# Optimization experiments

Hardware: AMD Instinct MI355X
Metric: run time of the kernel (lower is better)

## Reference

```python
import jax, jax.numpy as jnp
import numpy as np

EPS = 1e-6

def layer_norm(x, g, b):
    m = jnp.mean(x, axis=-1, keepdims=True)
    v = jnp.mean(jnp.square(x - m), axis=-1, keepdims=True)
    return (x - m) * jax.lax.rsqrt(v + EPS) * g + b

def setup_inputs() -> dict:
    key = jax.random.key(0)
    ks = jax.random.split(key, 12)
    B, L, D, Dff, SK = 8, 4096, 512, 2048, 128
    s = 0.02
    return {
        "x": jax.random.normal(ks[0], (B, L, D), jnp.float32),
        "Wq": jax.random.normal(ks[1], (D, D), jnp.float32) * s,
        "bq": jnp.zeros((D,), jnp.float32),
        "Wk": jax.random.normal(ks[2], (D, D), jnp.float32) * s,
        "bk": jnp.zeros((D,), jnp.float32),
        "Wv": jax.random.normal(ks[3], (D, D), jnp.float32) * s,
        "bv": jnp.zeros((D,), jnp.float32),
        "Wo": jax.random.normal(ks[4], (D, D), jnp.float32) * s,
        "bo": jnp.zeros((D,), jnp.float32),
        "g1": jnp.ones((D,), jnp.float32),
        "b1": jnp.zeros((D,), jnp.float32),
        "W1f": jax.random.normal(ks[5], (D, Dff), jnp.float32) * s,
        "b1f": jnp.zeros((Dff,), jnp.float32),
        "W2f": jax.random.normal(ks[6], (Dff, D), jnp.float32) * s,
        "b2f": jnp.zeros((D,), jnp.float32),
        "g2": jnp.ones((D,), jnp.float32),
        "b2": jnp.zeros((D,), jnp.float32),
        "sample_idx": jax.random.randint(ks[7], (SK,), 0, L, jnp.int64),
    }

NUM_HEADS = 8
TOP_U = 128

def prob_sparse_attention(x, Wq, bq, Wk, bk, Wv, bv, Wo, bo, sample_idx):
    B, L, D = x.shape
    H = NUM_HEADS
    dh = D // H
    scale = 1.0 / jnp.sqrt(jnp.asarray(dh, x.dtype))
    # projections -> [B, H, L, dh]
    def split_heads(t):
        return t.reshape(B, L, H, dh).transpose(0, 2, 1, 3)
    Q = split_heads(x @ Wq + bq)
    K = split_heads(x @ Wk + bk)
    V = split_heads(x @ Wv + bv)
    # sparsity measurement on a sampled key subset: [B, H, L, SK]
    K_samp = K[:, :, sample_idx, :]
    s_samp = jnp.einsum('bhld,bhsd->bhls', Q, K_samp)
    M = jnp.max(s_samp, axis=-1) - jnp.mean(s_samp, axis=-1)  # [B, H, L]
    _, top_idx = jax.lax.top_k(M, TOP_U)  # [B, H, u]
    # gather top-u queries: [B, H, u, dh]
    Q_top = jnp.take_along_axis(Q, top_idx[..., None], axis=2)
    scores = jnp.einsum('bhud,bhld->bhul', Q_top, K) * scale  # [B, H, u, L]
    attn = jax.nn.softmax(scores, axis=-1)
    ctx_top = jnp.einsum('bhul,bhld->bhud', attn, V)  # [B, H, u, dh]
    # lazy queries get mean(V)
    meanV = jnp.mean(V, axis=2, keepdims=True)  # [B, H, 1, dh]
    ctx = jnp.broadcast_to(meanV, (B, H, L, dh))
    bi = jnp.arange(B)[:, None, None]
    hi = jnp.arange(H)[None, :, None]
    ctx = ctx.at[bi, hi, top_idx].set(ctx_top)
    out = ctx.transpose(0, 2, 1, 3).reshape(B, L, D)
    return out @ Wo + bo

def reference(x, Wq, bq, Wk, bk, Wv, bv, Wo, bo, g1, b1, W1f, b1f, W2f, b2f, g2, b2, sample_idx):
    attn_out = prob_sparse_attention(x, Wq, bq, Wk, bk, Wv, bv, Wo, bo, sample_idx)
    x1 = layer_norm(x + attn_out, g1, b1)
    ffn = jax.nn.relu(x1 @ W1f + b1f) @ W2f + b2f
    return layer_norm(x1 + ffn, g2, b2)
```

## Files before the change

### kernel.cpp

```cpp
#include <hip/hip_runtime.h>
#include <hip/hip_bf16.h>

using bf16 = __hip_bfloat16;

constexpr int Bd  = 8;
constexpr int Ld  = 4096;
constexpr int Dd  = 512;
constexpr int Hd  = 8;
constexpr int DHd = 64;
constexpr int DFFd= 2048;
constexpr int Ud  = 128;
constexpr int MLd = Bd * Ld;
constexpr int KSd = 16;

typedef short          bf16x8 __attribute__((ext_vector_type(8)));
typedef unsigned short u16x8  __attribute__((ext_vector_type(8)));
typedef float          f32x4  __attribute__((ext_vector_type(4)));

__device__ __forceinline__ float bf2float(bf16 v) { return __bfloat162float(v); }

__device__ __forceinline__ float wred_sum(float v) {
    #pragma unroll
    for (int o = 32; o > 0; o >>= 1) v += __shfl_xor(v, o);
    return v;
}
__device__ __forceinline__ float wred_max(float v) {
    #pragma unroll
    for (int o = 32; o > 0; o >>= 1) v = fmaxf(v, __shfl_xor(v, o));
    return v;
}
__device__ __forceinline__ float scrub(float v) {
    return (fabsf(v) < 1e20f) ? v : 0.0f;
}
__device__ __forceinline__ short f2bs(float f) {
    bf16 h = __float2bfloat16(f);
    return *reinterpret_cast<short*>(&h);
}

__device__ __forceinline__ void gload_lds16(const bf16* g, bf16* lds_base) {
    __builtin_amdgcn_global_load_lds((const __attribute__((address_space(1))) void*)g,
                                     (__attribute__((address_space(3))) void*)lds_base,
                                     16, 0, 0);
}

__global__ void detect_kernel(const void* xraw, int* flags) {
    const unsigned short* u = (const unsigned short*)xraw;
    __shared__ int cnt;
    if (threadIdx.x == 0) cnt = 0;
    __syncthreads();
    int local = 0;
    for (int i = threadIdx.x; i < 1024; i += 256) {
        int e = (u[2 * i] >> 7) & 0xFF;
        if (e >= 96 && e <= 142) local++;
    }
    atomicAdd(&cnt, local);
    __syncthreads();
    if (threadIdx.x == 0) flags[0] = (cnt < 512) ? 1 : 0;
}

__global__ void conv_kernel(const void* raw, bf16* dst, int n, const int* flags) {
    int i = blockIdx.x * 256 + threadIdx.x;
    if (i >= n) return;
    if (flags[0]) dst[i] = __float2bfloat16(((const float*)raw)[i]);
    else          dst[i] = ((const bf16*)raw)[i];
}

__global__ void convT_kernel(const void* raw, bf16* dst, int K, int N, const int* flags) {
    __shared__ bf16 tile[32][33];
    const int k0 = blockIdx.y * 32, n0 = blockIdx.x * 32;
    const int tx = threadIdx.x & 31, ty = threadIdx.x >> 5;
    #pragma unroll
    for (int p = 0; p < 4; ++p) {
        int k = k0 + ty + p * 8, n = n0 + tx;
        float v = flags[0] ? ((const float*)raw)[(size_t)k * N + n]
                           : bf2float(((const bf16*)raw)[(size_t)k * N + n]);
        tile[ty + p * 8][tx] = __float2bfloat16(v);
    }
    __syncthreads();
    #pragma unroll
    for (int p = 0; p < 4; ++p) {
        int n = n0 + ty + p * 8, k = k0 + tx;
        dst[(size_t)n * K + k] = tile[tx][ty + p * 8];
    }
}

__global__ void zero_kernel(int* p, int n) {
    int i = blockIdx.x * 256 + threadIdx.x;
    if (i < n) p[i] = 0;
}

__global__ void idx_kernel(const void* raw, int* out) {
    const int* r32 = (const int*)raw;
    __shared__ int is64;
    int t = threadIdx.x;
    if (t == 0) is64 = 1;
    __syncthreads();
    if (t < 64 && r32[2 * t + 1] != 0) is64 = 0;
    __syncthreads();
    int v = is64 ? r32[2 * t] : r32[t];
    out[t] = min(max(v, 0), Ld - 1);
}

template<bool RELU>
__launch_bounds__(256)
__global__ void mfma_gemm(const bf16* __restrict__ X, const bf16* __restrict__ WT,
                          const bf16* __restrict__ bias, bf16* __restrict__ C,
                          int M, int N, int K)
{
    __shared__ bf16 As[128 * 64];
    __shared__ bf16 Bs[128 * 64];
    const int t = threadIdx.x;
    const int lane = t & 63, wave = t >> 6;
    const int wr = wave >> 1, wc = wave & 1;
    const int quad = lane >> 4, l15 = lane & 15;

    const int nwg = gridDim.x * gridDim.y;
    int wg = blockIdx.y * gridDim.x + blockIdx.x;
    if ((nwg & 7) == 0)
        wg = (wg & 7) * (nwg >> 3) + (wg >> 3);
    const int m0 = (wg / gridDim.x) * 128, n0 = (wg % gridDim.x) * 128;

    const int rseg = lane >> 3;
    const int cs   = (lane & 7) ^ rseg;

    f32x4 acc[4][4] = {};

    for (int k0 = 0; k0 < K; k0 += 64) {
        #pragma unroll
        for (int p = 0; p < 4; ++p) {
            const int sg = wave * 4 + p;
            const int r  = sg * 8 + rseg;
            gload_lds16(&X [(size_t)(m0 + r) * K + k0 + cs * 8], &As[sg * 512]);
            gload_lds16(&WT[(size_t)(n0 + r) * K + k0 + cs * 8], &Bs[sg * 512]);
        }
        __syncthreads();
        #pragma unroll
        for (int kk = 0; kk < 2; ++kk) {
            const int ch = ((kk * 4 + quad) ^ (l15 & 7)) * 8;
            bf16x8 a[4], b[4];
            #pragma unroll
            for (int i = 0; i < 4; ++i) {
                a[i] = *(const bf16x8*)&As[(wr * 64 + i * 16 + l15) * 64 + ch];
                b[i] = *(const bf16x8*)&Bs[(wc * 64 + i * 16 + l15) * 64 + ch];
            }
            #pragma unroll
            for (int i = 0; i < 4; ++i)
                #pragma unroll
                for (int j = 0; j < 4; ++j)
                    acc[i][j] = __builtin_amdgcn_mfma_f32_16x16x32_bf16(a[i], b[j], acc[i][j], 0, 0, 0);
        }
        __syncthreads();
    }
    #pragma unroll
    for (int j = 0; j < 4; ++j) {
        int n = n0 + wc * 64 + j * 16 + l15;
        float bi = bf2float(bias[n]);
        #pragma unroll
        for (int i = 0; i < 4; ++i) {
            #pragma unroll
            for (int r = 0; r < 4; ++r) {
                int m = m0 + wr * 64 + i * 16 + quad * 4 + r;
                float v = acc[i][j][r] + bi;
                if (RELU) v = fmaxf(v, 0.0f);
                C[(size_t)m * N + n] = __float2bfloat16(v);
            }
        }
    }
}

__launch_bounds__(256)
__global__ void m_kernel(const bf16* __restrict__ Q, const bf16* __restrict__ Kg,
                         const int* __restrict__ sidx, float* __restrict__ Mv)
{
    __shared__ __align__(16) short Qs[128 * 64];
    __shared__ __align__(16) short Ks[128 * 64];
    __shared__ int sidxs[128];

    const int t = threadIdx.x, lane = t & 63, w = t >> 6;
    const int l15 = lane & 15, quad = lane >> 4;
    const int l0 = blockIdx.x * 128;
    const int bh = blockIdx.y, b = bh >> 3, h = bh & 7;

    if (t < 128) sidxs[t] = sidx[t];
    __syncthreads();

    const int rseg = lane >> 3;
    const int cs   = (lane & 7) ^ rseg;
    #pragma unroll
    for (int sg4 = 0; sg4 < 4; ++sg4) {
        const int sg = w * 4 + sg4;
        const int r  = sg * 8 + rseg;
        gload_lds16(Q  + ((size_t)(b * Ld + l0 + r))    * Dd + h * 64 + cs * 8,
                    (bf16*)&Qs[sg * 512]);
        gload_lds16(Kg + ((size_t)(b * Ld + sidxs[r])) * Dd + h * 64 + cs * 8,
                    (bf16*)&Ks[sg * 512]);
    }
    __syncthreads();

    f32x4 s[2][8] = {};
    #pragma unroll
    for (int kk = 0; kk < 2; ++kk) {
        const int ch = ((kk * 4 + quad) ^ (l15 & 7)) * 8;
        bf16x8 qa[2], kb[8];
        #pragma unroll
        for (int mt = 0; mt < 2; ++mt)
            qa[mt] = *(const bf16x8*)&Qs[(w * 32 + mt * 16 + l15) * 64 + ch];
        #pragma unroll
        for (int nt = 0; nt < 8; ++nt)
            kb[nt] = *(const bf16x8*)&Ks[(nt * 16 + l15) * 64 + ch];
        #pragma unroll
        for (int mt = 0; mt < 2; ++mt)
            #pragma unroll
            for (int nt = 0; nt < 8; ++nt)
                s[mt][nt] = __builtin_amdgcn_mfma_f32_16x16x32_bf16(qa[mt], kb[nt], s[mt][nt], 0, 0, 0);
    }

    #pragma unroll
    for (int mt = 0; mt < 2; ++mt) {
        #pragma unroll
        for (int r = 0; r < 4; ++r) {
            float vmax = -1e30f, vsum = 0.0f;
            #pragma unroll
            for (int nt = 0; nt < 8; ++nt) {
                float v = s[mt][nt][r];
                vmax = fmaxf(vmax, v); vsum += v;
            }
            #pragma unroll
            for (int off = 1; off < 16; off <<= 1) {
                vmax = fmaxf(vmax, __shfl_xor(vmax, off));
                vsum += __shfl_xor(vsum, off);
            }
            if (l15 == 0) {
                const int row = w * 32 + mt * 16 + quad * 4 + r;
                Mv[(size_t)bh * Ld + l0 + row] = vmax - vsum * (1.0f / 128.0f);
            }
        }
    }
}

__launch_bounds__(256)
__global__ void topk_kernel(const float* __restrict__ Mv, int* __restrict__ topIdx)
{
    __shared__ unsigned ukey[4096];
    __shared__ short listA[4096], listB[4096];
    __shared__ int hist[256];
    __shared__ int outCnt, candCnt, selB, aboveK;
    const int bh = blockIdx.x, t = threadIdx.x;

    for (int i = t; i < 4096; i += 256) {
        unsigned u = __float_as_uint(Mv[(size_t)bh * Ld + i]);
        ukey[i] = (u & 0x80000000u) ? ~u : (u | 0x80000000u);
    }
    if (t == 0) outCnt = 0;
    __syncthreads();

    int K = Ud;
    #pragma unroll
    for (int r = 0; r < 4; ++r) {
        const int shift = 24 - 8 * r;
        hist[t] = 0;
        __syncthreads();
        const int n = (r == 0) ? 4096 : candCnt;
        const short* cur = (r & 1) ? listB : listA;
        for (int i = t; i < n; i += 256) {
            int idx = (r == 0) ? i : cur[i];
            atomicAdd(&hist[(ukey[idx] >> shift) & 0xFF], 1);
        }
        __syncthreads();
        if (t == 0) {
            int cum = 0, b = 255;
            for (; b > 0; --b) {
                if (cum + hist[b] >= K) break;
                cum += hist[b];
            }
            selB = b; aboveK = cum; candCnt = 0;
        }
        __syncthreads();
        const int sb = selB;
        short* nxt = (r & 1) ? listA : listB;
        for (int i = t; i < n; i += 256) {
            int idx = (r == 0) ? i : cur[i];
            int by = (ukey[idx] >> shift) & 0xFF;
            if (by > sb) {
                int p = atomicAdd(&outCnt, 1);
                topIdx[bh * Ud + p] = idx;
            } else if (by == sb) {
                int p = atomicAdd(&candCnt, 1);
                nxt[p] = (short)idx;
            }
        }
        __syncthreads();
        K -= aboveK;
        if (K == 0) break;
    }
    if (K > 0) {
        for (int i = t; i < K; i += 256) {
            int p = atomicAdd(&outCnt, 1);
            topIdx[bh * Ud + p] = listA[i];
        }
    }
}

__global__ void rows_kernel(const int* __restrict__ topIdx, int* __restrict__ rowCnt,
                            int* __restrict__ rowEnt)
{
    const int bh = blockIdx.x, u = threadIdx.x, b = bh >> 3;
    const int lq = topIdx[bh * Ud + u];
    const int row = b * Ld + lq;
    int slot = atomicAdd(&rowCnt[row], 1) & 7;
    rowEnt[row * 8 + slot] = bh * Ud + u;
}

__launch_bounds__(256)
__global__ void meanv_kernel(const bf16* __restrict__ V, float* __restrict__ meanV)
{
    const int bh = blockIdx.x, b = bh >> 3, h = bh & 7;
    const int l0 = blockIdx.y * 64;
    const int t = threadIdx.x;
    const int d = t & 63, part = t >> 6;
    float s = 0.0f;
    #pragma unroll
    for (int p = 0; p < 16; ++p) {
        int l = l0 + part + p * 4;
        s += bf2float(V[((size_t)(b * Ld + l)) * Dd + h * 64 + d]);
    }
    __shared__ float red[256];
    red[t] = s;
    __syncthreads();
    if (t < 64) {
        float tot = red[t] + red[64 + t] + red[128 + t] + red[192 + t];
        atomicAdd(&meanV[bh * 64 + t], tot * (1.0f / 4096.0f));
    }
}

__launch_bounds__(256, 3)
__global__ void attn_kernel(const bf16* __restrict__ Qg, const bf16* __restrict__ Kg,
                            const bf16* __restrict__ Vg, const int* __restrict__ topIdx,
                            bf16* __restrict__ pO, float* __restrict__ pM, float* __restrict__ pL)
{
    __shared__ __align__(16) short KsS[2][64 * 64];
    __shared__ __align__(16) short VsS[2][64 * 72];
    __shared__ __align__(16) short PsS[4][32 * 72];

    const int t = threadIdx.x, lane = t & 63, w = t >> 6;
    const int l15 = lane & 15, quad = lane >> 4;
    const int bh = blockIdx.x, ks = blockIdx.y;
    const int b = bh >> 3, h = bh & 7;
    const int key0 = ks * (Ld / KSd);
    constexpr int NT = (Ld / KSd) / 64;

    bf16x8 qf[2][2];
    #pragma unroll
    for (int m = 0; m < 2; ++m) {
        const int u  = w * 32 + m * 16 + l15;
        const int lq = topIdx[bh * Ud + u];
        const bf16* qr = Qg + ((size_t)(b * Ld + lq)) * Dd + h * 64;
        qf[m][0] = *(const bf16x8*)(qr + quad * 8);
        qf[m][1] = *(const bf16x8*)(qr + 32 + quad * 8);
    }

    const int vkey = t >> 2, vd0 = (t & 3) * 16;
    u16x8 vr0, vr1;

    auto loadV = [&](int tt) {
        const bf16* vs = Vg + ((size_t)(b * Ld + key0 + tt * 64 + vkey)) * Dd + h * 64 + vd0;
        vr0 = *(const u16x8*)vs;
        vr1 = *(const u16x8*)(vs + 8);
    };
    auto stageK = [&](int buf, int tt) {
        const int kb0 = key0 + tt * 64;
        #pragma unroll
        for (int sz = 0; sz < 2; ++sz) {
            const int sg = w * 2 + sz;
            const int r  = sg * 8 + (lane >> 3);
            const int cs = (lane & 7) ^ (lane >> 3);
            gload_lds16(Kg + ((size_t)(b * Ld + kb0 + r)) * Dd + h * 64 + cs * 8,
                        (bf16*)&KsS[buf][sg * 512]);
        }
    };
    auto writeV = [&](int buf) {
        #pragma unroll
        for (int j = 0; j < 8; ++j) {
            VsS[buf][(vd0 + j) * 72 + vkey]     = (short)vr0[j];
            VsS[buf][(vd0 + 8 + j) * 72 + vkey] = (short)vr1[j];
        }
    };

    float mrun[2][4], lrun[2][4];
    f32x4 o[2][4] = {};
    #pragma unroll
    for (int m = 0; m < 2; ++m)
        #pragma unroll
        for (int r = 0; r < 4; ++r) { mrun[m][r] = -1e30f; lrun[m][r] = 0.0f; }

    loadV(0); stageK(0, 0); writeV(0);
    __syncthreads();

    short* PsW = &PsS[w][0];
    for (int tt = 0; tt < NT; ++tt) {
        const int cur = tt & 1;
        if (tt + 1 < NT) { loadV(tt + 1); stageK(cur ^ 1, tt + 1); }

        const short* KsB = &KsS[cur][0];
        f32x4 s[2][4] = {};
        #pragma unroll
        for (int kk = 0; kk < 2; ++kk) {
            bf16x8 kb[4];
            #pragma unroll
            for (int n = 0; n < 4; ++n)
                kb[n] = *(const bf16x8*)&KsB[(n * 16 + l15) * 64 +
                                             (((kk * 4 + quad) ^ (l15 & 7)) * 8)];
            #pragma unroll
            for (int m = 0; m < 2; ++m)
                #pragma unroll
                for (int n = 0; n < 4; ++n)
                    s[m][n] = __builtin_amdgcn_mfma_f32_16x16x32_bf16(qf[m][kk], kb[n], s[m][n], 0, 0, 0);
        }

        #pragma unroll
        for (int m = 0; m < 2; ++m) {
            #pragma unroll
            for (int r = 0; r < 4; ++r) {
                float sv[4];
                #pragma unroll
                for (int n = 0; n < 4; ++n) sv[n] = s[m][n][r] * 0.125f;
                float vm = fmaxf(fmaxf(sv[0], sv[1]), fmaxf(sv[2], sv[3]));
                #pragma unroll
                for (int off = 1; off < 16; off <<= 1) vm = fmaxf(vm, __shfl_xor(vm, off));
                const float mn = fmaxf(mrun[m][r], vm);
                const float al = __expf(mrun[m][r] - mn);
                float ps = 0.0f;
                #pragma unroll
                for (int n = 0; n < 4; ++n) { sv[n] = __expf(sv[n] - mn); ps += sv[n]; }
                #pragma unroll
                for (int off = 1; off < 16; off <<= 1) ps += __shfl_xor(ps, off);
                lrun[m][r] = lrun[m][r] * al + ps;
                mrun[m][r] = mn;
                const int qrow = m * 16 + quad * 4 + r;
                #pragma unroll
                for (int n = 0; n < 4; ++n) {
                    PsW[qrow * 72 + n * 16 + l15] = f2bs(sv[n]);
                    o[m][n][r] *= al;
                }
            }
        }

        if (tt + 1 < NT) writeV(cur ^ 1);

        const short* VsB = &VsS[cur][0];
        #pragma unroll
        for (int kk = 0; kk < 2; ++kk) {
            bf16x8 pa[2], vb[4];
            #pragma unroll
            for (int m = 0; m < 2; ++m)
                pa[m] = *(const bf16x8*)&PsW[(m * 16 + l15) * 72 + kk * 32 + quad * 8];
            #pragma unroll
            for (int n = 0; n < 4; ++n)
                vb[n] = *(const bf16x8*)&VsB[(n * 16 + l15) * 72 + kk * 32 + quad * 8];
            #pragma unroll
            for (int m = 0; m < 2; ++m)
                #pragma unroll
                for (int n = 0; n < 4; ++n)
                    o[m][n] = __builtin_amdgcn_mfma_f32_16x16x32_bf16(pa[m], vb[n], o[m][n], 0, 0, 0);
        }
        __syncthreads();
    }

    const size_t pbase = ((size_t)(ks * 64 + bh)) * Ud;
    #pragma unroll
    for (int m = 0; m < 2; ++m) {
        #pragma unroll
        for (int r = 0; r < 4; ++r) {
            const int u = w * 32 + m * 16 + quad * 4 + r;
            #pragma unroll
            for (int n = 0; n < 4; ++n)
                pO[(pbase + u) * 64 + n * 16 + l15] = __float2bfloat16(o[m][n][r]);
            if (l15 == 0) { pM[pbase + u] = mrun[m][r]; pL[pbase + u] = lrun[m][r]; }
        }
    }
}

__global__ void combine_kernel(const bf16* __restrict__ pO, const float* __restrict__ pM,
                               const float* __restrict__ pL, float* __restrict__ ctxTop)
{
    const int u = blockIdx.x & 127, bh = blockIdx.x >> 7, c = threadIdx.x;
    float mstar = -1e30f;
    #pragma unroll
    for (int ks = 0; ks < KSd; ++ks)
        mstar = fmaxf(mstar, pM[(ks * 64 + bh) * Ud + u]);
    float lsum = 0.0f, osum = 0.0f;
    #pragma unroll
    for (int ks = 0; ks < KSd; ++ks) {
        float wgt = __expf(pM[(ks * 64 + bh) * Ud + u] - mstar);
        lsum += pL[(ks * 64 + bh) * Ud + u] * wgt;
        osum += bf2float(pO[(((size_t)ks * 64 + bh) * Ud + u) * 64 + c]) * wgt;
    }
    ctxTop[((size_t)bh * Ud + u) * 64 + c] = scrub(osum / lsum);
}

__launch_bounds__(512)
__global__ void baseout_kernel(const float* __restrict__ meanV, const bf16* __restrict__ Wo,
                               const bf16* __restrict__ bo, float* __restrict__ baseOut)
{
    const int b = blockIdx.x, t = threadIdx.x;
    __shared__ float mv[512];
    mv[t] = meanV[b * 512 + t];
    __syncthreads();
    float acc = bf2float(bo[t]);
    for (int d = 0; d < 512; ++d)
        acc = fmaf(mv[d], bf2float(Wo[(size_t)d * 512 + t]), acc);
    baseOut[b * 512 + t] = acc;
}

__launch_bounds__(256)
__global__ void delta_kernel(const float* __restrict__ ctxTop, const float* __restrict__ meanV,
                             const bf16* __restrict__ Wo, bf16* __restrict__ deltaOut)
{
    const int u = blockIdx.x, bh = blockIdx.y, h = bh & 7, t = threadIdx.x;
    __shared__ float diff[64];
    if (t < 64) diff[t] = ctxTop[((size_t)bh * Ud + u) * 64 + t] - meanV[bh * 64 + t];
    __syncthreads();
    for (int n = t; n < 512; n += 256) {
        float acc = 0.0f;
        #pragma unroll 8
        for (int dd = 0; dd < 64; ++dd)
            acc = fmaf(diff[dd], bf2float(Wo[(size_t)(h * 64 + dd) * 512 + n]), acc);
        deltaOut[((size_t)bh * Ud + u) * 512 + n] = __float2bfloat16(acc);
    }
}

__launch_bounds__(256)
__global__ void ln1_kernel(const bf16* __restrict__ x, const float* __restrict__ baseOut,
                           const int* __restrict__ rowCnt, const int* __restrict__ rowEnt,
                           const bf16* __restrict__ deltaOut,
                           const bf16* __restrict__ g, const bf16* __restrict__ bb,
                           bf16* __restrict__ x1)
{
    const int row = blockIdx.x, t = threadIdx.x;
    const int b = row >> 12;
    const size_t base = (size_t)row * 512;
    float v0 = bf2float(x[base + t])       + baseOut[b * 512 + t];
    float v1 = bf2float(x[base + t + 256]) + baseOut[b * 512 + t + 256];
    const int cnt = min(rowCnt[row], 8);
    for (int e = 0; e < cnt; ++e) {
        const bf16* dr = &deltaOut[(size_t)rowEnt[row * 8 + e] * 512];
        v0 += bf2float(dr[t]);
        v1 += bf2float(dr[t + 256]);
    }
    v0 = scrub(v0); v1 = scrub(v1);
    float s = v0 + v1, q = v0 * v0 + v1 * v1;
    s = wred_sum(s); q = wred_sum(q);
    __shared__ float sred[4], qred[4];
    int lane = t & 63, w = t >> 6;
    if (lane == 0) { sred[w] = s; qred[w] = q; }
    __syncthreads();
    float tot  = sred[0] + sred[1] + sred[2] + sred[3];
    float totq = qred[0] + qred[1] + qred[2] + qred[3];
    float mean = tot * (1.0f / 512.0f);
    float var  = fmaxf(totq * (1.0f / 512.0f) - mean * mean, 0.0f);
    float rstd = rsqrtf(var + 1e-6f);
    x1[base + t]       = __float2bfloat16((v0 - mean) * rstd * bf2float(g[t])       + bf2float(bb[t]));
    x1[base + t + 256] = __float2bfloat16((v1 - mean) * rstd * bf2float(g[t + 256]) + bf2float(bb[t + 256]));
}

__launch_bounds__(256)
__global__ void ln2_kernel(const bf16* __restrict__ x1, const bf16* __restrict__ ffn,
                           const bf16* __restrict__ g, const bf16* __restrict__ bb,
                           void* __restrict__ out, const int* __restrict__ flags)
{
    const int row = blockIdx.x, t = threadIdx.x;
    const size_t base = (size_t)row * 512;
    float v0 = bf2float(x1[base + t])       + bf2float(ffn[base + t]);
    float v1 = bf2float(x1[base + t + 256]) + bf2float(ffn[base + t + 256]);
    v0 = scrub(v0); v1 = scrub(v1);
    float s = v0 + v1, q = v0 * v0 + v1 * v1;
    s = wred_sum(s); q = wred_sum(q);
    __shared__ float sred[4], qred[4];
    int lane = t & 63, w = t >> 6;
    if (lane == 0) { sred[w] = s; qred[w] = q; }
    __syncthreads();
    float tot  = sred[0] + sred[1] + sred[2] + sred[3];
    float totq = qred[0] + qred[1] + qred[2] + qred[3];
    float mean = tot * (1.0f / 512.0f);
    float var  = fmaxf(totq * (1.0f / 512.0f) - mean * mean, 0.0f);
    float rstd = rsqrtf(var + 1e-6f);
    float o0 = (v0 - mean) * rstd * bf2float(g[t])       + bf2float(bb[t]);
    float o1 = (v1 - mean) * rstd * bf2float(g[t + 256]) + bf2float(bb[t + 256]);
    if (flags[0]) {
        ((float*)out)[base + t]       = o0;
        ((float*)out)[base + t + 256] = o1;
    } else {
        ((bf16*)out)[base + t]       = __float2bfloat16(o0);
        ((bf16*)out)[base + t + 256] = __float2bfloat16(o1);
    }
}

extern "C" void kernel_launch(void* const* d_in, const int* in_sizes, int n_in,
                              void* d_out, int out_size, void* d_ws, size_t ws_size,
                              hipStream_t stream)
{
    const void* sraw = d_in[17];

    const size_t NQ = (size_t)MLd * Dd;
    char* w = (char*)d_ws;
    size_t off = 0;
    auto alloc = [&](size_t bytes) { void* p = w + off; off += (bytes + 63) & ~size_t(63); return p; };
    bf16*  Qb   = (bf16*)alloc(NQ * 2);
    bf16*  Kb   = (bf16*)alloc(NQ * 2);
    bf16*  Vb   = (bf16*)alloc(NQ * 2);
    bf16*  xc   = (bf16*)alloc(NQ * 2);
    bf16*  WTq  = (bf16*)alloc(Dd * Dd * 2);
    bf16*  WTk  = (bf16*)alloc(Dd * Dd * 2);
    bf16*  WTv  = (bf16*)alloc(Dd * Dd * 2);
    bf16*  Woc  = (bf16*)alloc(Dd * Dd * 2);
    bf16*  WT1f = (bf16*)alloc((size_t)Dd * DFFd * 2);
    bf16*  WT2f = (bf16*)alloc((size_t)DFFd * Dd * 2);
    bf16* bqc = (bf16*)alloc(Dd * 2);
    bf16* bkc = (bf16*)alloc(Dd * 2);
    bf16* bvc = (bf16*)alloc(Dd * 2);
    bf16* boc = (bf16*)alloc(Dd * 2);
    bf16* g1c = (bf16*)alloc(Dd * 2);
    bf16* b1c = (bf16*)alloc(Dd * 2);
    bf16* b1fc= (bf16*)alloc(DFFd * 2);
    bf16* b2fc= (bf16*)alloc(Dd * 2);
    bf16* g2c = (bf16*)alloc(Dd * 2);
    bf16* b2c = (bf16*)alloc(Dd * 2);
    bf16*  pOb     = (bf16*)alloc((size_t)KSd * 64 * Ud * 64 * 2);
    float* Mv      = (float*)alloc((size_t)Bd * Hd * Ld * 4);
    float* ctxTop  = (float*)alloc((size_t)Bd * Hd * Ud * DHd * 4);
    float* meanV   = (float*)alloc(Bd * Hd * DHd * 4);
    float* baseOut = (float*)alloc(Bd * Dd * 4);
    int*   topIdx  = (int*)alloc(Bd * Hd * Ud * 4);
    int*   sidx    = (int*)alloc(128 * 4);
    int*   rowCnt  = (int*)alloc(MLd * 4);
    int*   rowEnt  = (int*)alloc(MLd * 8 * 4);
    int*   flags   = (int*)alloc(64);
    if (off > ws_size) return;

    bf16* h1full = nullptr;
    if (ws_size - off >= (size_t)MLd * DFFd * 2 + 64)
        h1full = (bf16*)alloc((size_t)MLd * DFFd * 2);

    bf16*  x1b  = Vb;
    bf16*  h1b  = Qb;
    bf16*  ffnb = xc;
    bf16*  deltaOut = pOb;
    float* pM = Mv;
    float* pL = Mv + KSd * 64 * Ud;

    detect_kernel<<<1, 256, 0, stream>>>(d_in[0], flags);

    auto conv = [&](int i, bf16* dst, int n) {
        conv_kernel<<<(n + 255) / 256, 256, 0, stream>>>(d_in[i], dst, n, flags);
    };
    conv(0,  xc, (int)NQ);
    convT_kernel<<<dim3(Dd / 32, Dd / 32), 256, 0, stream>>>(d_in[1], WTq, Dd, Dd, flags);
    convT_kernel<<<dim3(Dd / 32, Dd / 32), 256, 0, stream>>>(d_in[3], WTk, Dd, Dd, flags);
    convT_kernel<<<dim3(Dd / 32, Dd / 32), 256, 0, stream>>>(d_in[5], WTv, Dd, Dd, flags);
    convT_kernel<<<dim3(DFFd / 32, Dd / 32), 256, 0, stream>>>(d_in[11], WT1f, Dd, DFFd, flags);
    convT_kernel<<<dim3(Dd / 32, DFFd / 32), 256, 0, stream>>>(d_in[13], WT2f, DFFd, Dd, flags);
    conv(7,  Woc, Dd * Dd);
    conv(2,  bqc, Dd);  conv(4,  bkc, Dd);  conv(6,  bvc, Dd);  conv(8,  boc, Dd);
    conv(9,  g1c, Dd);  conv(10, b1c, Dd);
    conv(12, b1fc, DFFd); conv(14, b2fc, Dd);
    conv(15, g2c, Dd);  conv(16, b2c, Dd);

    zero_kernel<<<(MLd + 255) / 256, 256, 0, stream>>>(rowCnt, MLd);
    zero_kernel<<<(Bd * Hd * DHd + 255) / 256, 256, 0, stream>>>((int*)meanV, Bd * Hd * DHd);
    idx_kernel<<<1, 128, 0, stream>>>(sraw, sidx);

    mfma_gemm<false><<<dim3(4, 256), 256, 0, stream>>>(xc, WTq, bqc, Qb, MLd, Dd, Dd);
    mfma_gemm<false><<<dim3(4, 256), 256, 0, stream>>>(xc, WTk, bkc, Kb, MLd, Dd, Dd);
    mfma_gemm<false><<<dim3(4, 256), 256, 0, stream>>>(xc, WTv, bvc, Vb, MLd, Dd, Dd);

    m_kernel<<<dim3(Ld / 128, Bd * Hd), 256, 0, stream>>>(Qb, Kb, sidx, Mv);
    topk_kernel<<<Bd * Hd, 256, 0, stream>>>(Mv, topIdx);
    rows_kernel<<<Bd * Hd, 128, 0, stream>>>(topIdx, rowCnt, rowEnt);
    meanv_kernel<<<dim3(Bd * Hd, Ld / 64), 256, 0, stream>>>(Vb, meanV);

    attn_kernel<<<dim3(Bd * Hd, KSd), 256, 0, stream>>>(Qb, Kb, Vb, topIdx, pOb, pM, pL);
    combine_kernel<<<Bd * Hd * Ud, 64, 0, stream>>>(pOb, pM, pL, ctxTop);

    baseout_kernel<<<Bd, 512, 0, stream>>>(meanV, Woc, boc, baseOut);
    delta_kernel<<<dim3(Ud, Bd * Hd), 256, 0, stream>>>(ctxTop, meanV, Woc, deltaOut);

    ln1_kernel<<<MLd, 256, 0, stream>>>(xc, baseOut, rowCnt, rowEnt, deltaOut, g1c, b1c, x1b);

    if (h1full) {
        mfma_gemm<true ><<<dim3(16, 256), 256, 0, stream>>>(x1b, WT1f, b1fc, h1full, MLd, DFFd, Dd);
        mfma_gemm<false><<<dim3(4, 256), 256, 0, stream>>>(h1full, WT2f, b2fc, ffnb, MLd, Dd, DFFd);
    } else {
        for (int c = 0; c < 2; ++c) {
            mfma_gemm<true ><<<dim3(16, 128), 256, 0, stream>>>(
                x1b + (size_t)c * 16384 * 512, WT1f, b1fc, h1b, 16384, DFFd, Dd);
            mfma_gemm<false><<<dim3(4, 128), 256, 0, stream>>>(
                h1b, WT2f, b2fc, ffnb + (size_t)c * 16384 * 512, 16384, Dd, DFFd);
        }
    }

    ln2_kernel<<<MLd, 256, 0, stream>>>(x1b, ffnb, g2c, b2c, d_out, flags);
}
```

Baseline: 695.4 us.

## Double-buffer GEMM LDS tiles, fuse QKV projections, widen combine blocks

```diff
diff --git a/kernel.cpp b/kernel.cpp
--- a/kernel.cpp
+++ b/kernel.cpp
@@ -101,14 +101,14 @@
     out[t] = min(max(v, 0), Ld - 1);
 }
 
-template<bool RELU>
+template<bool RELU, bool QKV3>
 __launch_bounds__(256)
 __global__ void mfma_gemm(const bf16* __restrict__ X, const bf16* __restrict__ WT,
                           const bf16* __restrict__ bias, bf16* __restrict__ C,
                           int M, int N, int K)
 {
-    __shared__ bf16 As[128 * 64];
-    __shared__ bf16 Bs[128 * 64];
+    __shared__ bf16 As[2][128 * 64];
+    __shared__ bf16 Bs[2][128 * 64];
     const int t = threadIdx.x;
     const int lane = t & 63, wave = t >> 6;
     const int wr = wave >> 1, wc = wave & 1;
@@ -123,25 +123,32 @@
     const int rseg = lane >> 3;
     const int cs   = (lane & 7) ^ rseg;
 
-    f32x4 acc[4][4] = {};
-
-    for (int k0 = 0; k0 < K; k0 += 64) {
+    auto stage = [&](int buf, int k0) {
         #pragma unroll
         for (int p = 0; p < 4; ++p) {
             const int sg = wave * 4 + p;
             const int r  = sg * 8 + rseg;
-            gload_lds16(&X [(size_t)(m0 + r) * K + k0 + cs * 8], &As[sg * 512]);
-            gload_lds16(&WT[(size_t)(n0 + r) * K + k0 + cs * 8], &Bs[sg * 512]);
-        }
-        __syncthreads();
+            gload_lds16(&X [(size_t)(m0 + r) * K + k0 + cs * 8], &As[buf][sg * 512]);
+            gload_lds16(&WT[(size_t)(n0 + r) * K + k0 + cs * 8], &Bs[buf][sg * 512]);
+        }
+    };
+
+    f32x4 acc[4][4] = {};
+
+    stage(0, 0);
+    __syncthreads();
+    int cur = 0;
+    const int NI = K >> 6;
+    for (int it = 0; it < NI; ++it) {
+        if (it + 1 < NI) stage(cur ^ 1, (it + 1) << 6);
         #pragma unroll
         for (int kk = 0; kk < 2; ++kk) {
             const int ch = ((kk * 4 + quad) ^ (l15 & 7)) * 8;
             bf16x8 a[4], b[4];
             #pragma unroll
             for (int i = 0; i < 4; ++i) {
-                a[i] = *(const bf16x8*)&As[(wr * 64 + i * 16 + l15) * 64 + ch];
-                b[i] = *(const bf16x8*)&Bs[(wc * 64 + i * 16 + l15) * 64 + ch];
+                a[i] = *(const bf16x8*)&As[cur][(wr * 64 + i * 16 + l15) * 64 + ch];
+                b[i] = *(const bf16x8*)&Bs[cur][(wc * 64 + i * 16 + l15) * 64 + ch];
             }
             #pragma unroll
             for (int i = 0; i < 4; ++i)
@@ -149,12 +156,22 @@
                 for (int j = 0; j < 4; ++j)
                     acc[i][j] = __builtin_amdgcn_mfma_f32_16x16x32_bf16(a[i], b[j], acc[i][j], 0, 0, 0);
         }
-        __syncthreads();
+        if (it + 1 < NI) __syncthreads();
+        cur ^= 1;
     }
     #pragma unroll
     for (int j = 0; j < 4; ++j) {
         int n = n0 + wc * 64 + j * 16 + l15;
         float bi = bf2float(bias[n]);
+        bf16* cb;
+        size_t stride;
+        if (QKV3) {
+            cb = C + (size_t)(n >> 9) * ((size_t)MLd * Dd) + (n & (Dd - 1));
+            stride = Dd;
+        } else {
+            cb = C + n;
+            stride = (size_t)N;
+        }
         #pragma unroll
         for (int i = 0; i < 4; ++i) {
             #pragma unroll
@@ -162,7 +179,7 @@
                 int m = m0 + wr * 64 + i * 16 + quad * 4 + r;
                 float v = acc[i][j][r] + bi;
                 if (RELU) v = fmaxf(v, 0.0f);
-                C[(size_t)m * N + n] = __float2bfloat16(v);
+                cb[(size_t)m * stride] = __float2bfloat16(v);
             }
         }
     }
@@ -480,10 +497,12 @@
     }
 }
 
+__launch_bounds__(256)
 __global__ void combine_kernel(const bf16* __restrict__ pO, const float* __restrict__ pM,
                                const float* __restrict__ pL, float* __restrict__ ctxTop)
 {
-    const int u = blockIdx.x & 127, bh = blockIdx.x >> 7, c = threadIdx.x;
+    const int t = threadIdx.x, c = t & 63, ui = t >> 6;
+    const int u = (blockIdx.x & 31) * 4 + ui, bh = blockIdx.x >> 5;
     float mstar = -1e30f;
     #pragma unroll
     for (int ks = 0; ks < KSd; ++ks)
@@ -669,9 +688,7 @@
     zero_kernel<<<(Bd * Hd * DHd + 255) / 256, 256, 0, stream>>>((int*)meanV, Bd * Hd * DHd);
     idx_kernel<<<1, 128, 0, stream>>>(sraw, sidx);
 
-    mfma_gemm<false><<<dim3(4, 256), 256, 0, stream>>>(xc, WTq, bqc, Qb, MLd, Dd, Dd);
-    mfma_gemm<false><<<dim3(4, 256), 256, 0, stream>>>(xc, WTk, bkc, Kb, MLd, Dd, Dd);
-    mfma_gemm<false><<<dim3(4, 256), 256, 0, stream>>>(xc, WTv, bvc, Vb, MLd, Dd, Dd);
+    mfma_gemm<false, true><<<dim3(12, 256), 256, 0, stream>>>(xc, WTq, bqc, Qb, MLd, 3 * Dd, Dd);
 
     m_kernel<<<dim3(Ld / 128, Bd * Hd), 256, 0, stream>>>(Qb, Kb, sidx, Mv);
     topk_kernel<<<Bd * Hd, 256, 0, stream>>>(Mv, topIdx);
@@ -679,7 +696,7 @@
     meanv_kernel<<<dim3(Bd * Hd, Ld / 64), 256, 0, stream>>>(Vb, meanV);
 
     attn_kernel<<<dim3(Bd * Hd, KSd), 256, 0, stream>>>(Qb, Kb, Vb, topIdx, pOb, pM, pL);
-    combine_kernel<<<Bd * Hd * Ud, 64, 0, stream>>>(pOb, pM, pL, ctxTop);
+    combine_kernel<<<Bd * Hd * 32, 256, 0, stream>>>(pOb, pM, pL, ctxTop);
 
     baseout_kernel<<<Bd, 512, 0, stream>>>(meanV, Woc, boc, baseOut);
     delta_kernel<<<dim3(Ud, Bd * Hd), 256, 0, stream>>>(ctxTop, meanV, Woc, deltaOut);
@@ -687,13 +704,13 @@
     ln1_kernel<<<MLd, 256, 0, stream>>>(xc, baseOut, rowCnt, rowEnt, deltaOut, g1c, b1c, x1b);
 
     if (h1full) {
-        mfma_gemm<true ><<<dim3(16, 256), 256, 0, stream>>>(x1b, WT1f, b1fc, h1full, MLd, DFFd, Dd);
-        mfma_gemm<false><<<dim3(4, 256), 256, 0, stream>>>(h1full, WT2f, b2fc, ffnb, MLd, Dd, DFFd);
+        mfma_gemm<true , false><<<dim3(16, 256), 256, 0, stream>>>(x1b, WT1f, b1fc, h1full, MLd, DFFd, Dd);
+        mfma_gemm<false, false><<<dim3(4, 256), 256, 0, stream>>>(h1full, WT2f, b2fc, ffnb, MLd, Dd, DFFd);
     } else {
         for (int c = 0; c < 2; ++c) {
-            mfma_gemm<true ><<<dim3(16, 128), 256, 0, stream>>>(
+            mfma_gemm<true , false><<<dim3(16, 128), 256, 0, stream>>>(
                 x1b + (size_t)c * 16384 * 512, WT1f, b1fc, h1b, 16384, DFFd, Dd);
-            mfma_gemm<false><<<dim3(4, 128), 256, 0, stream>>>(
+            mfma_gemm<false, false><<<dim3(4, 128), 256, 0, stream>>>(
                 h1b, WT2f, b2fc, ffnb + (size_t)c * 16384 * 512, 16384, Dd, DFFd);
         }
     }
```

Measured after the change: 669.0 us. 1.04x faster.
